# Performance work log

Hardware: AMD Instinct MI355X
Metric: run time of the kernel (lower is better)

Reference implementation:

```python
import jax, jax.numpy as jnp
import numpy as np

IN_CH = 31
OUT_CH = 31
G = 5          # grid_size
K = 3          # spline_order
GRID_LO, GRID_HI = -1.0, 1.0
NB = G + K     # number of B-spline basis functions
COEF_LEN = IN_CH * OUT_CH * NB        # 7688
UNIV_LEN = IN_CH * OUT_CH             # 961
RES_LEN = IN_CH * OUT_CH              # 961
PARAMS = COEF_LEN + UNIV_LEN + RES_LEN  # 9610


def _b_splines(x):
    """Cox-de Boor B-spline bases. x: (N, IN_CH) -> (N, IN_CH, G+K)."""
    h = (GRID_HI - GRID_LO) / G
    grid = jnp.arange(-K, G + K + 1, dtype=x.dtype) * h + GRID_LO  # (G+2K+1,)
    xe = x[..., None]
    b = ((xe >= grid[:-1]) & (xe < grid[1:])).astype(x.dtype)  # order-0, (N,I,G+2K)
    for p in range(1, K + 1):
        b = ((xe - grid[:-(p + 1)]) / (grid[p:-1] - grid[:-(p + 1)])) * b[..., :-1] \
          + ((grid[p + 1:] - xe) / (grid[p + 1:] - grid[1:-p])) * b[..., 1:]
    return b  # (N, IN_CH, NB)


def setup_inputs() -> dict:
    key = jax.random.key(0)
    k1, k2, k3 = jax.random.split(key, 3)
    # x in [-1,1) to span grid_range
    x = jax.random.uniform(k1, (1, IN_CH, 128, 128), dtype=jnp.float32) * 2.0 - 1.0
    # hypernetwork (generator) params: 3x3 conv 31 -> 9610
    gen_w = jax.random.normal(k2, (PARAMS, IN_CH, 3, 3), dtype=jnp.float32) * 0.02
    gen_b = jax.random.normal(k3, (PARAMS,), dtype=jnp.float32) * 0.01
    return {"x": x, "gen_w": gen_w, "gen_b": gen_b}


def reference(x, gen_w, gen_b):
    B, C, H, W = x.shape
    # generator: per-pixel KAN parameters, (B, PARAMS, H, W)
    w = jax.lax.conv_general_dilated(
        x, gen_w, window_strides=(1, 1), padding='SAME',
        dimension_numbers=('NCHW', 'OIHW', 'NCHW')) + gen_b[None, :, None, None]
    w = jnp.transpose(w, (0, 2, 3, 1)).reshape(B * H * W, PARAMS)
    xf = jnp.transpose(x, (0, 2, 3, 1)).reshape(B * H * W, C)
    # slice per-pixel params (mirrors kan_params_indices slicing + view)
    coef = w[:, :COEF_LEN].reshape(-1, IN_CH, OUT_CH, NB)
    univ = w[:, COEF_LEN:COEF_LEN + UNIV_LEN].reshape(-1, IN_CH, OUT_CH)
    res = w[:, COEF_LEN + UNIV_LEN:].reshape(-1, IN_CH, OUT_CH)
    bases = _b_splines(xf)                                # (N, I, NB)
    spline = jnp.einsum('nid,niod->nio', bases, coef)     # per-edge spline value
    silu = xf * jax.nn.sigmoid(xf)                        # residual activation
    out = jnp.einsum('nio,nio->no', univ, spline) + jnp.einsum('ni,nio->no', silu, res)
    return jnp.transpose(out.reshape(B, H, W, OUT_CH), (0, 3, 1, 2))
```

## Files before the change

kernel.cpp:

```cpp
#include <hip/hip_runtime.h>
#include <hip/hip_bf16.h>

#define OUT_CH   31
#define COEF_LEN 7688
#define NPIX     16384
#define CHUNKS   31
#define NFRG     24
#define NR       9
#define FRAG_U16 512
#define STEP_U16 (NFRG*FRAG_U16)
#define BP3_B    ((size_t)CHUNKS*NR*STEP_U16*2)
#define P1_B     ((size_t)OUT_CH*NPIX*4)
#define WS_NEED  (BP3_B + P1_B)

#define SLAB_OFF  0
#define WT_OFF    24960
#define SLT_OFF   92544
#define LDS_BYTES 97664

using f32x4 = __attribute__((ext_vector_type(4))) float;
using s16x8 = __attribute__((ext_vector_type(8))) short;

__device__ __forceinline__ unsigned short f2bf(float f) {
    unsigned int u = __float_as_uint(f);
    unsigned int r = (u + 0x7FFFu + ((u >> 16) & 1u)) >> 16;
    return (unsigned short)r;
}

__global__ void pack_kernel(const float* __restrict__ gw, const float* __restrict__ gb,
                            unsigned short* __restrict__ bp) {
    const int NMAIN = CHUNKS * NFRG * 64;
    int tt = blockIdx.x * 256 + threadIdx.x;
    if (tt >= NMAIN) return;
    int lane = tt & 63;
    int u = tt >> 6;
    int f = u % NFRG;
    int i = u / NFRG;
    int m = lane & 15, q8 = lane >> 4;
    int o = (m >> 2) * 8 + f / 3;
    int jslot = (f % 3) * 4 + (m & 3);
    int p = -1;
    if (o < OUT_CH && jslot < 10) {
        if (jslot < 8)       p = i * 248 + o * 8 + jslot;
        else if (jslot == 8) p = COEF_LEN + i * 31 + o;
        else                 p = COEF_LEN + 961 + i * 31 + o;
    }
    s16x8 vr[NR];
    #pragma unroll
    for (int r = 0; r < NR; ++r)
        #pragma unroll
        for (int jj = 0; jj < 8; ++jj) vr[r][jj] = 0;
    #pragma unroll
    for (int jj = 0; jj < 8; ++jj) {
        int ci = q8 * 8 + jj;
        if (p >= 0) {
            if (ci < 31) {
                const float* gr = gw + (long)p * 279 + ci * 9;
                #pragma unroll
                for (int r = 0; r < NR; ++r) vr[r][jj] = (short)f2bf(gr[r]);
            } else {
                vr[4][jj] = (short)f2bf(gb[p]);
            }
        }
    }
    #pragma unroll
    for (int r = 0; r < NR; ++r)
        *reinterpret_cast<s16x8*>(bp + (((size_t)i * NR + r) * NFRG + f) * FRAG_U16 + lane * 8) = vr[r];
}

__global__ void __launch_bounds__(1024, 1)
main_kernel(const float* __restrict__ x, const unsigned short* __restrict__ bp3,
            float* __restrict__ dst0, float* __restrict__ dst1,
            int two_cg, int c0_in, int nc_in, int add_in) {
    extern __shared__ char smem[];
    unsigned short* slab = (unsigned short*)(smem + SLAB_OFF);
    float* Wt = (float*)(smem + WT_OFF);
    unsigned short* SLt = (unsigned short*)(smem + SLT_OFF);

    const int tid = threadIdx.x;
    const int bid = blockIdx.x;
    int row, c0, nc, addf;
    float* dst;
    if (two_cg) {
        int cg = bid & 1;
        row = bid >> 1;
        c0 = cg ? 16 : 0;
        nc = cg ? 15 : 16;
        dst = cg ? dst1 : dst0;
        addf = 0;
    } else {
        row = bid;
        c0 = c0_in; nc = nc_in; dst = dst0; addf = add_in;
    }

    for (int idx = tid; idx < 3 * 130 * 32; idx += 1024) {
        int slot = idx & 31;
        int rix = idx >> 5;
        int cc = rix % 130;
        int rr = rix / 130;
        int hh = row - 1 + rr, ww = cc - 1;
        unsigned short v = 0;
        if (slot < 31) {
            if ((unsigned)hh < 128u && (unsigned)ww < 128u)
                v = f2bf(x[slot * NPIX + hh * 128 + ww]);
        } else {
            v = 0x3F80;
        }
        slab[rix * 32 + (((slot >> 3) ^ (rix & 3)) << 3) + (slot & 7)] = v;
    }

    for (int idx = tid; idx < nc * 128; idx += 1024) {
        int px = idx & 127;
        int k = idx >> 7;
        float xv = x[(size_t)(c0 + k) * NPIX + row * 128 + px];
        float u5 = (xv + 1.0f) * 2.5f;
        float cf = fminf(fmaxf(floorf(u5), 0.f), 4.f);
        int ccb = (int)cf;
        float t = u5 - cf;
        float omt = 1.f - t;
        float t2v = t * t, t3v = t2v * t;
        float bw0 = omt * omt * omt * (1.f / 6.f);
        float bw3 = t3v * (1.f / 6.f);
        float bw1 = 0.5f * t3v - t2v + (2.f / 3.f);
        float bw2 = 1.f - bw0 - bw1 - bw3;
        float* wr = Wt + px * 132 + k * 8;
        *reinterpret_cast<f32x4*>(wr) = (f32x4){0.f, 0.f, 0.f, 0.f};
        *reinterpret_cast<f32x4*>(wr + 4) = (f32x4){0.f, 0.f, 0.f, 0.f};
        wr[ccb] = bw0; wr[ccb + 1] = bw1; wr[ccb + 2] = bw2; wr[ccb + 3] = bw3;
        SLt[px * 20 + k] = f2bf(xv / (1.f + __expf(-xv)));
    }
    __syncthreads();

    const int lane = tid & 63;
    const int w = tid >> 6;
    const int fi = w & 7;
    const int ph = w >> 3;
    const int q = lane >> 4;
    const int pix16 = lane & 15;
    const char* slabb = (const char*)slab;

    const int rb3 = pix16 & 3;
    int swzt[4];
    #pragma unroll
    for (int c = 0; c < 4; ++c)
        swzt[c] = (q ^ ((rb3 + c) & 3)) << 4;
    int rb64[4];
    #pragma unroll
    for (int pg = 0; pg < 4; ++pg)
        rb64[pg] = (ph * 64 + pg * 16 + pix16) * 64;

    float oreg[4] = {0.f, 0.f, 0.f, 0.f};

    #pragma unroll 1
    for (int k = 0; k < nc; ++k) {
        const unsigned short* aw = bp3
            + ((size_t)(c0 + k) * NR * NFRG + fi * 3) * FRAG_U16 + lane * 8;

        s16x8 pa[2][3];
        #pragma unroll
        for (int fl = 0; fl < 3; ++fl)
            pa[0][fl] = *reinterpret_cast<const s16x8*>(aw + fl * FRAG_U16);

        f32x4 acc[3][4];
        #pragma unroll
        for (int fl = 0; fl < 3; ++fl)
            #pragma unroll
            for (int pg = 0; pg < 4; ++pg)
                acc[fl][pg] = (f32x4){0.f, 0.f, 0.f, 0.f};

        #pragma unroll
        for (int r = 0; r < NR; ++r) {
            if (r + 1 < NR) {
                #pragma unroll
                for (int fl = 0; fl < 3; ++fl)
                    pa[(r + 1) & 1][fl] = *reinterpret_cast<const s16x8*>(
                        aw + (r + 1) * STEP_U16 + fl * FRAG_U16);
            }
            const int cr = (r / 3) * 130 + (r % 3);
            s16x8 pbv[4];
            #pragma unroll
            for (int pg = 0; pg < 4; ++pg)
                pbv[pg] = *reinterpret_cast<const s16x8*>(
                    slabb + rb64[pg] + cr * 64 + swzt[cr & 3]);

            __builtin_amdgcn_s_setprio(1);
            #pragma unroll
            for (int fl = 0; fl < 3; ++fl)
                #pragma unroll
                for (int pg = 0; pg < 4; ++pg)
                    acc[fl][pg] = __builtin_amdgcn_mfma_f32_16x16x32_bf16(
                        pa[r & 1][fl], pbv[pg], acc[fl][pg], 0, 0, 0);
            __builtin_amdgcn_s_setprio(0);
        }

        #pragma unroll
        for (int pg = 0; pg < 4; ++pg) {
            const int px = ph * 64 + pg * 16 + pix16;
            const float* wr = Wt + px * 132 + k * 8;
            f32x4 wlo = *reinterpret_cast<const f32x4*>(wr);
            f32x4 whi = *reinterpret_cast<const f32x4*>(wr + 4);
            unsigned short slb = SLt[px * 20 + k];
            float sl = __uint_as_float((unsigned)slb << 16);
            float sp = wlo[0] * acc[0][pg][0];
            sp = fmaf(wlo[1], acc[0][pg][1], sp);
            sp = fmaf(wlo[2], acc[0][pg][2], sp);
            sp = fmaf(wlo[3], acc[0][pg][3], sp);
            sp = fmaf(whi[0], acc[1][pg][0], sp);
            sp = fmaf(whi[1], acc[1][pg][1], sp);
            sp = fmaf(whi[2], acc[1][pg][2], sp);
            sp = fmaf(whi[3], acc[1][pg][3], sp);
            oreg[pg] = fmaf(acc[2][pg][0], sp, fmaf(sl, acc[2][pg][1], oreg[pg]));
        }
    }

    const int o = q * 8 + fi;
    if (o < OUT_CH) {
        #pragma unroll
        for (int pg = 0; pg < 4; ++pg) {
            size_t gi = (size_t)o * NPIX + row * 128 + ph * 64 + pg * 16 + pix16;
            if (addf) dst[gi] += oreg[pg];
            else      dst[gi]  = oreg[pg];
        }
    }
}

__global__ void reduce_kernel(const float* __restrict__ p1, float* __restrict__ out) {
    int e = blockIdx.x * 256 + threadIdx.x;
    if (e < OUT_CH * NPIX) out[e] += p1[e];
}

extern "C" void kernel_launch(void* const* d_in, const int* in_sizes, int n_in,
                              void* d_out, int out_size, void* d_ws, size_t ws_size,
                              hipStream_t stream) {
    const float* x  = (const float*)d_in[0];
    const float* gw = (const float*)d_in[1];
    const float* gb = (const float*)d_in[2];
    float* outp = (float*)d_out;
    unsigned short* bpack = (unsigned short*)d_ws;
    float* p1 = (float*)((char*)d_ws + BP3_B);

    hipFuncSetAttribute((const void*)main_kernel,
                        hipFuncAttributeMaxDynamicSharedMemorySize, LDS_BYTES);

    const int NMAIN = CHUNKS * NFRG * 64;
    pack_kernel<<<(NMAIN + 255) / 256, 256, 0, stream>>>(gw, gb, bpack);

    if (ws_size >= WS_NEED) {
        main_kernel<<<256, 1024, LDS_BYTES, stream>>>(x, bpack, outp, p1, 1, 0, 0, 0);
        reduce_kernel<<<(OUT_CH * NPIX + 255) / 256, 256, 0, stream>>>(p1, outp);
    } else {
        main_kernel<<<128, 1024, LDS_BYTES, stream>>>(x, bpack, outp, nullptr, 0, 0, 16, 0);
        main_kernel<<<128, 1024, LDS_BYTES, stream>>>(x, bpack, outp, nullptr, 0, 16, 15, 1);
    }
}
```

Baseline: 106.9 us.

## Switch generator GEMM to 32x32x16 MFMA with repacked weight tiles

Replaces the 16x16x32 bf16 MFMA tiling with 32x32x16 MFMA tiles, repacking the generator weights into 12 tiles over 18 K-steps per input channel and remapping output channels across the tile rows. Each wave now covers 32 pixels and 3 tiles instead of 64 pixels and 3 fragments, and it double-buffers the LDS B-operand loads alongside the global A loads. The goal is fewer LDS reads and instructions per FLOP via the larger MFMA shape, plus a simpler epilogue. The cost is a more complex output-channel mapping and a pack kernel that now loops over steps.

```diff
diff --git a/kernel.cpp b/kernel.cpp
--- a/kernel.cpp
+++ b/kernel.cpp
@@ -5,21 +5,21 @@
 #define COEF_LEN 7688
 #define NPIX     16384
 #define CHUNKS   31
-#define NFRG     24
-#define NR       9
-#define FRAG_U16 512
-#define STEP_U16 (NFRG*FRAG_U16)
-#define BP3_B    ((size_t)CHUNKS*NR*STEP_U16*2)
+#define NTILE    12
+#define NS       18
+#define TILE_U16 512
+#define BP4_B    ((size_t)CHUNKS*NS*NTILE*TILE_U16*2)
 #define P1_B     ((size_t)OUT_CH*NPIX*4)
-#define WS_NEED  (BP3_B + P1_B)
+#define WS_NEED  (BP4_B + P1_B)
 
 #define SLAB_OFF  0
 #define WT_OFF    24960
 #define SLT_OFF   92544
 #define LDS_BYTES 97664
 
-using f32x4 = __attribute__((ext_vector_type(4))) float;
-using s16x8 = __attribute__((ext_vector_type(8))) short;
+using f32x4  = __attribute__((ext_vector_type(4))) float;
+using f32x16 = __attribute__((ext_vector_type(16))) float;
+using s16x8  = __attribute__((ext_vector_type(8))) short;
 
 __device__ __forceinline__ unsigned short f2bf(float f) {
     unsigned int u = __float_as_uint(f);
@@ -29,47 +29,44 @@
 
 __global__ void pack_kernel(const float* __restrict__ gw, const float* __restrict__ gb,
                             unsigned short* __restrict__ bp) {
-    const int NMAIN = CHUNKS * NFRG * 64;
+    const int NMAIN = CHUNKS * NTILE * 64;
     int tt = blockIdx.x * 256 + threadIdx.x;
     if (tt >= NMAIN) return;
     int lane = tt & 63;
-    int u = tt >> 6;
-    int f = u % NFRG;
-    int i = u / NFRG;
-    int m = lane & 15, q8 = lane >> 4;
-    int o = (m >> 2) * 8 + f / 3;
-    int jslot = (f % 3) * 4 + (m & 3);
+    int t = (tt >> 6) % NTILE;
+    int i = (tt >> 6) / NTILE;
+    int m = lane & 31, l5 = lane >> 5;
+    int g = m >> 3, l5m = (m >> 2) & 1, r03 = m & 3;
+    int o, js;
+    if (g < 3) { o = 2 * t + l5m;           js = 4 * g + r03; }
+    else       { o = 24 + 2 * (t / 3) + l5m; js = 4 * (t % 3) + r03; }
     int p = -1;
-    if (o < OUT_CH && jslot < 10) {
-        if (jslot < 8)       p = i * 248 + o * 8 + jslot;
-        else if (jslot == 8) p = COEF_LEN + i * 31 + o;
-        else                 p = COEF_LEN + 961 + i * 31 + o;
-    }
-    s16x8 vr[NR];
-    #pragma unroll
-    for (int r = 0; r < NR; ++r)
-        #pragma unroll
-        for (int jj = 0; jj < 8; ++jj) vr[r][jj] = 0;
-    #pragma unroll
-    for (int jj = 0; jj < 8; ++jj) {
-        int ci = q8 * 8 + jj;
-        if (p >= 0) {
-            if (ci < 31) {
-                const float* gr = gw + (long)p * 279 + ci * 9;
-                #pragma unroll
-                for (int r = 0; r < NR; ++r) vr[r][jj] = (short)f2bf(gr[r]);
-            } else {
-                vr[4][jj] = (short)f2bf(gb[p]);
+    if (o < OUT_CH && js < 10) {
+        if (js < 8)       p = i * 248 + o * 8 + js;
+        else if (js == 8) p = COEF_LEN + i * 31 + o;
+        else              p = COEF_LEN + 961 + i * 31 + o;
+    }
+    #pragma unroll 1
+    for (int s = 0; s < NS; ++s) {
+        int r = s >> 1;
+        int ci0 = 16 * (s & 1) + 8 * l5;
+        s16x8 v;
+        #pragma unroll
+        for (int jj = 0; jj < 8; ++jj) {
+            int ci = ci0 + jj;
+            float val = 0.f;
+            if (p >= 0) {
+                if (ci < 31)            val = gw[(long)p * 279 + ci * 9 + r];
+                else if (r == 4)        val = gb[p];
             }
-        }
-    }
-    #pragma unroll
-    for (int r = 0; r < NR; ++r)
-        *reinterpret_cast<s16x8*>(bp + (((size_t)i * NR + r) * NFRG + f) * FRAG_U16 + lane * 8) = vr[r];
+            v[jj] = (short)f2bf(val);
+        }
+        *reinterpret_cast<s16x8*>(bp + (((size_t)i * NS + s) * NTILE + t) * TILE_U16 + lane * 8) = v;
+    }
 }
 
 __global__ void __launch_bounds__(1024, 1)
-main_kernel(const float* __restrict__ x, const unsigned short* __restrict__ bp3,
+main_kernel(const float* __restrict__ x, const unsigned short* __restrict__ bp4,
             float* __restrict__ dst0, float* __restrict__ dst1,
             int two_cg, int c0_in, int nc_in, int add_in) {
     extern __shared__ char smem[];
@@ -133,93 +130,106 @@
 
     const int lane = tid & 63;
     const int w = tid >> 6;
-    const int fi = w & 7;
-    const int ph = w >> 3;
-    const int q = lane >> 4;
-    const int pix16 = lane & 15;
+    const int fi = w & 3;
+    const int xq = w >> 2;
+    const int l5 = lane >> 5;
+    const int n32 = lane & 31;
+    const int n = xq * 32 + n32;
     const char* slabb = (const char*)slab;
 
-    const int rb3 = pix16 & 3;
-    int swzt[4];
+    int rbc[4];
     #pragma unroll
-    for (int c = 0; c < 4; ++c)
-        swzt[c] = (q ^ ((rb3 + c) & 3)) << 4;
-    int rb64[4];
-    #pragma unroll
-    for (int pg = 0; pg < 4; ++pg)
-        rb64[pg] = (ph * 64 + pg * 16 + pix16) * 64;
+    for (int c = 0; c < 4; ++c) rbc[c] = ((lane & 3) + c) & 3;
+    const int nrow = n * 64;
 
     float oreg[4] = {0.f, 0.f, 0.f, 0.f};
 
     #pragma unroll 1
     for (int k = 0; k < nc; ++k) {
-        const unsigned short* aw = bp3
-            + ((size_t)(c0 + k) * NR * NFRG + fi * 3) * FRAG_U16 + lane * 8;
+        const int ic = c0 + k;
+        const unsigned short* awc = bp4
+            + ((size_t)ic * NS * NTILE + 3 * fi) * TILE_U16 + lane * 8;
 
         s16x8 pa[2][3];
         #pragma unroll
-        for (int fl = 0; fl < 3; ++fl)
-            pa[0][fl] = *reinterpret_cast<const s16x8*>(aw + fl * FRAG_U16);
-
-        f32x4 acc[3][4];
-        #pragma unroll
-        for (int fl = 0; fl < 3; ++fl)
+        for (int tl = 0; tl < 3; ++tl)
+            pa[0][tl] = *reinterpret_cast<const s16x8*>(awc + tl * TILE_U16);
+
+        s16x8 pbv[2];
+        pbv[0] = *reinterpret_cast<const s16x8*>(
+            slabb + nrow + ((l5 ^ rbc[0]) << 4));
+
+        f32x16 acc[3];
+        #pragma unroll
+        for (int tl = 0; tl < 3; ++tl)
             #pragma unroll
-            for (int pg = 0; pg < 4; ++pg)
-                acc[fl][pg] = (f32x4){0.f, 0.f, 0.f, 0.f};
-
-        #pragma unroll
-        for (int r = 0; r < NR; ++r) {
-            if (r + 1 < NR) {
+            for (int e = 0; e < 16; ++e) acc[tl][e] = 0.f;
+
+        #pragma unroll
+        for (int s = 0; s < NS; ++s) {
+            if (s + 1 < NS) {
                 #pragma unroll
-                for (int fl = 0; fl < 3; ++fl)
-                    pa[(r + 1) & 1][fl] = *reinterpret_cast<const s16x8*>(
-                        aw + (r + 1) * STEP_U16 + fl * FRAG_U16);
+                for (int tl = 0; tl < 3; ++tl)
+                    pa[(s + 1) & 1][tl] = *reinterpret_cast<const s16x8*>(
+                        awc + ((s + 1) * NTILE + tl) * TILE_U16);
+                const int sn = s + 1;
+                const int rn = sn >> 1;
+                const int crn = (rn / 3) * 130 + (rn % 3);
+                const int c2n = 2 * (sn & 1) + l5;
+                pbv[(s + 1) & 1] = *reinterpret_cast<const s16x8*>(
+                    slabb + nrow + crn * 64 + ((c2n ^ rbc[crn & 3]) << 4));
             }
-            const int cr = (r / 3) * 130 + (r % 3);
-            s16x8 pbv[4];
-            #pragma unroll
-            for (int pg = 0; pg < 4; ++pg)
-                pbv[pg] = *reinterpret_cast<const s16x8*>(
-                    slabb + rb64[pg] + cr * 64 + swzt[cr & 3]);
-
             __builtin_amdgcn_s_setprio(1);
             #pragma unroll
-            for (int fl = 0; fl < 3; ++fl)
-                #pragma unroll
-                for (int pg = 0; pg < 4; ++pg)
-                    acc[fl][pg] = __builtin_amdgcn_mfma_f32_16x16x32_bf16(
-                        pa[r & 1][fl], pbv[pg], acc[fl][pg], 0, 0, 0);
+            for (int tl = 0; tl < 3; ++tl)
+                acc[tl] = __builtin_amdgcn_mfma_f32_32x32x16_bf16(
+                    pa[s & 1][tl], pbv[s & 1], acc[tl], 0, 0, 0);
             __builtin_amdgcn_s_setprio(0);
         }
 
-        #pragma unroll
-        for (int pg = 0; pg < 4; ++pg) {
-            const int px = ph * 64 + pg * 16 + pix16;
-            const float* wr = Wt + px * 132 + k * 8;
-            f32x4 wlo = *reinterpret_cast<const f32x4*>(wr);
-            f32x4 whi = *reinterpret_cast<const f32x4*>(wr + 4);
-            unsigned short slb = SLt[px * 20 + k];
-            float sl = __uint_as_float((unsigned)slb << 16);
-            float sp = wlo[0] * acc[0][pg][0];
-            sp = fmaf(wlo[1], acc[0][pg][1], sp);
-            sp = fmaf(wlo[2], acc[0][pg][2], sp);
-            sp = fmaf(wlo[3], acc[0][pg][3], sp);
-            sp = fmaf(whi[0], acc[1][pg][0], sp);
-            sp = fmaf(whi[1], acc[1][pg][1], sp);
-            sp = fmaf(whi[2], acc[1][pg][2], sp);
-            sp = fmaf(whi[3], acc[1][pg][3], sp);
-            oreg[pg] = fmaf(acc[2][pg][0], sp, fmaf(sl, acc[2][pg][1], oreg[pg]));
-        }
-    }
-
-    const int o = q * 8 + fi;
-    if (o < OUT_CH) {
-        #pragma unroll
-        for (int pg = 0; pg < 4; ++pg) {
-            size_t gi = (size_t)o * NPIX + row * 128 + ph * 64 + pg * 16 + pix16;
-            if (addf) dst[gi] += oreg[pg];
-            else      dst[gi]  = oreg[pg];
+        const float* wr = Wt + n * 132 + k * 8;
+        f32x4 wlo = *reinterpret_cast<const f32x4*>(wr);
+        f32x4 whi = *reinterpret_cast<const f32x4*>(wr + 4);
+        unsigned short slb = SLt[n * 20 + k];
+        float sl = __uint_as_float((unsigned)slb << 16);
+        #pragma unroll
+        for (int tl = 0; tl < 3; ++tl) {
+            float sp = wlo[0] * acc[tl][0];
+            sp = fmaf(wlo[1], acc[tl][1], sp);
+            sp = fmaf(wlo[2], acc[tl][2], sp);
+            sp = fmaf(wlo[3], acc[tl][3], sp);
+            sp = fmaf(whi[0], acc[tl][4], sp);
+            sp = fmaf(whi[1], acc[tl][5], sp);
+            sp = fmaf(whi[2], acc[tl][6], sp);
+            sp = fmaf(whi[3], acc[tl][7], sp);
+            oreg[tl] = fmaf(acc[tl][8], sp, fmaf(sl, acc[tl][9], oreg[tl]));
+        }
+        {
+            float sp = wlo[0] * acc[0][12];
+            sp = fmaf(wlo[1], acc[0][13], sp);
+            sp = fmaf(wlo[2], acc[0][14], sp);
+            sp = fmaf(wlo[3], acc[0][15], sp);
+            sp = fmaf(whi[0], acc[1][12], sp);
+            sp = fmaf(whi[1], acc[1][13], sp);
+            sp = fmaf(whi[2], acc[1][14], sp);
+            sp = fmaf(whi[3], acc[1][15], sp);
+            oreg[3] = fmaf(acc[2][12], sp, fmaf(sl, acc[2][13], oreg[3]));
+        }
+    }
+
+    #pragma unroll
+    for (int tl = 0; tl < 3; ++tl) {
+        const int o = 6 * fi + 2 * tl + l5;
+        size_t gi = (size_t)o * NPIX + row * 128 + n;
+        if (addf) dst[gi] += oreg[tl];
+        else      dst[gi]  = oreg[tl];
+    }
+    {
+        const int o = 24 + 2 * fi + l5;
+        if (o < OUT_CH) {
+            size_t gi = (size_t)o * NPIX + row * 128 + n;
+            if (addf) dst[gi] += oreg[3];
+            else      dst[gi]  = oreg[3];
         }
     }
 }
@@ -237,12 +247,12 @@
     const float* gb = (const float*)d_in[2];
     float* outp = (float*)d_out;
     unsigned short* bpack = (unsigned short*)d_ws;
-    float* p1 = (float*)((char*)d_ws + BP3_B);
+    float* p1 = (float*)((char*)d_ws + BP4_B);
 
     hipFuncSetAttribute((const void*)main_kernel,
                         hipFuncAttributeMaxDynamicSharedMemorySize, LDS_BYTES);
 
-    const int NMAIN = CHUNKS * NFRG * 64;
+    const int NMAIN = CHUNKS * NTILE * 64;
     pack_kernel<<<(NMAIN + 255) / 256, 256, 0, stream>>>(gw, gb, bpack);
 
     if (ws_size >= WS_NEED) {
```

Measured after the change: 157.0 us. 46.9% more time.
